# Kernel optimization log

Hardware: AMD Instinct MI355X
Metric: run time of the kernel (lower is better)

Reference implementation:

```python
import jax, jax.numpy as jnp
import numpy as np

N = 32          # agents_num
IN_DIM = 16     # node feature dim (excluding 2 pos cols)
HID = 128
HEADS = 4
OUT = 5
DUEL_H = 256
RADIUS = 0.3
LATENT = HID + HID * HEADS * 2  # 1152
BS = 128


def _lin(k, i, o):
    s = 1.0 / np.sqrt(i)
    return jax.random.uniform(k, (i, o), minval=-s, maxval=s, dtype=jnp.float32)


def setup_inputs() -> dict:
    key = jax.random.key(0)
    ks = jax.random.split(key, 16)
    pos = jax.random.uniform(ks[0], (BS, N, 2))
    feats = jax.random.normal(ks[1], (BS, N, IN_DIM))
    aidx = jax.random.randint(ks[2], (BS,), 0, N).astype(jnp.float32)
    node = jnp.concatenate([pos, feats], axis=-1).reshape(BS, N * (2 + IN_DIM))
    obs = jnp.concatenate([node, aidx[:, None]], axis=1)  # (BS, N*(2+IN_DIM)+1)
    return {
        "obs": obs,
        "enc_w1": _lin(ks[3], IN_DIM, HID), "enc_b1": jnp.zeros((HID,)),
        "enc_w2": _lin(ks[4], HID, HID), "enc_b2": jnp.zeros((HID,)),
        "wl1": _lin(ks[5], HID, HEADS * HID), "wr1": _lin(ks[6], HID, HEADS * HID),
        "att1": jax.random.normal(ks[7], (HEADS, HID)) * 0.1, "bias1": jnp.zeros((HEADS * HID,)),
        "wl2": _lin(ks[8], HID * HEADS, HEADS * HID), "wr2": _lin(ks[9], HID * HEADS, HEADS * HID),
        "att2": jax.random.normal(ks[10], (HEADS, HID)) * 0.1, "bias2": jnp.zeros((HEADS * HID,)),
        "q_w1": _lin(ks[11], LATENT, DUEL_H), "q_b1": jnp.zeros((DUEL_H,)),
        "q_w2": _lin(ks[12], DUEL_H, OUT), "q_b2": jnp.zeros((OUT,)),
        "v_w1": _lin(ks[13], LATENT, DUEL_H), "v_b1": jnp.zeros((DUEL_H,)),
        "v_w2": _lin(ks[14], DUEL_H, 1), "v_b2": jnp.zeros((1,)),
    }


def _gatv2(x, adj, wl, wr, att, bias):
    # Dense-masked GATv2 (PyG semantics: lin_l on source j, lin_r on target i,
    # leaky_relu(x_i + x_j) . att, softmax over neighbors j, aggregate lin_l(x_j)).
    bs, n, _ = x.shape
    gl = (x @ wl).reshape(bs, n, HEADS, HID)  # source transform
    gr = (x @ wr).reshape(bs, n, HEADS, HID)  # target transform
    e = jax.nn.leaky_relu(gr[:, :, None] + gl[:, None, :], 0.2)  # [b, i, j, h, c]
    logits = jnp.einsum('bijhc,hc->bijh', e, att)
    logits = jnp.where(adj[..., None], logits, -jnp.inf)  # diag always True (self loops)
    alpha = jax.nn.softmax(logits, axis=2)
    out = jnp.einsum('bijh,bjhc->bihc', alpha, gl).reshape(bs, n, HEADS * HID)
    return out + bias


def reference(obs, enc_w1, enc_b1, enc_w2, enc_b2,
              wl1, wr1, att1, bias1, wl2, wr2, att2, bias2,
              q_w1, q_b1, q_w2, q_b2, v_w1, v_b1, v_w2, v_b2):
    bs = obs.shape[0]
    node = obs[:, :-1].reshape(bs, N, 2 + IN_DIM)
    pos, feats = node[..., :2], node[..., 2:]
    aidx = jnp.clip(obs[:, -1], 0, N - 1).astype(jnp.int32)

    # radius_graph (per-graph, loop=False) + GATv2 add_self_loops => diag True
    d2 = jnp.sum((pos[:, :, None] - pos[:, None, :]) ** 2, axis=-1)  # [bs, N, N]
    adj = (d2 < RADIUS ** 2) | jnp.eye(N, dtype=bool)

    # encoder MLP then ReLU (as in forward)
    h = jax.nn.relu(feats @ enc_w1 + enc_b1)
    x = jax.nn.relu(h @ enc_w2 + enc_b2)  # [bs, N, HID]

    b = jnp.arange(bs)
    x1 = x[b, aidx]  # [bs, HID]

    x = jax.nn.relu(_gatv2(x, adj, wl1, wr1, att1, bias1))  # [bs, N, HID*HEADS]
    x2 = x[b, aidx]

    x = jax.nn.relu(_gatv2(x, adj, wl2, wr2, att2, bias2))
    x3 = x[b, aidx]

    x_cat = jnp.concatenate([x1, x2, x3], axis=1)  # [bs, LATENT]

    q = jax.nn.relu(x_cat @ q_w1 + q_b1) @ q_w2 + q_b2  # [bs, OUT]
    v = jax.nn.relu(x_cat @ v_w1 + v_b1) @ v_w2 + v_b2  # [bs, 1]
    return q - q.mean(axis=1, keepdims=True) + v
```

## Files before the change

kernel.cpp:

```cpp
#include <hip/hip_runtime.h>
#include <hip/hip_bf16.h>

typedef unsigned int uint_t;
typedef unsigned short ushort_t;
typedef __attribute__((ext_vector_type(8))) short short8;
typedef __attribute__((ext_vector_type(4))) float floatx4;

__device__ __forceinline__ float4 fma4(float4 a, float s, float4 w){
  a.x += s*w.x; a.y += s*w.y; a.z += s*w.z; a.w += s*w.w; return a;
}
__device__ __forceinline__ float4 relu4(float4 a){
  return make_float4(fmaxf(a.x,0.f),fmaxf(a.y,0.f),fmaxf(a.z,0.f),fmaxf(a.w,0.f));
}
__device__ __forceinline__ float comp4(float4 v, int k){
  return k==0? v.x : k==1? v.y : k==2? v.z : v.w;
}
__device__ __forceinline__ unsigned bf16rne(float f){
  unsigned u = __float_as_uint(f);
  return (u + 0x7fffu + ((u>>16)&1u)) >> 16;
}
__device__ __forceinline__ uint_t packbf(float f){
  unsigned hb = bf16rne(f);
  float hf = __uint_as_float(hb<<16);
  unsigned lb = bf16rne(f - hf);
  return (hb<<16) | lb;
}
__device__ __forceinline__ uint4 pack4(float4 v){
  uint4 u; u.x=packbf(v.x); u.y=packbf(v.y); u.z=packbf(v.z); u.w=packbf(v.w); return u;
}
__device__ __forceinline__ float unpk(uint_t u){
  return __uint_as_float(u & 0xffff0000u) + __uint_as_float(u<<16);
}


__global__ __launch_bounds__(256) void prep_kernel(
    const float* __restrict__ obs,
    const float* __restrict__ enc_w1, const float* __restrict__ enc_b1,
    const float* __restrict__ enc_w2, const float* __restrict__ enc_b2,
    const float* __restrict__ wl1, const float* __restrict__ wr1,
    const float* __restrict__ wl2,
    const float* __restrict__ q_w1, const float* __restrict__ v_w1,
    ushort_t* __restrict__ wl1Thi, ushort_t* __restrict__ wl1Tlo,
    ushort_t* __restrict__ wr1Thi, ushort_t* __restrict__ wr1Tlo,
    ushort_t* __restrict__ wl2Thi, ushort_t* __restrict__ wl2Tlo,
    ushort_t* __restrict__ qw1Thi, ushort_t* __restrict__ qw1Tlo,
    ushort_t* __restrict__ vw1Thi, ushort_t* __restrict__ vw1Tlo,
    uint_t* __restrict__ xpk,
    uint_t* __restrict__ xcatpk,
    unsigned* __restrict__ adjw, int* __restrict__ aiw)
{
  const int t = threadIdx.x, bid = blockIdx.x;
  if (bid >= 512){
    __shared__ float sm[32][33];
    const int cw = bid - 512;
    const float* in; ushort_t* ohi; ushort_t* olo; int K, N, tt;
    if (cw < 64)        { in=wl1;  ohi=wl1Thi; olo=wl1Tlo; K=128;  N=512; tt=cw; }
    else if (cw < 128)  { in=wr1;  ohi=wr1Thi; olo=wr1Tlo; K=128;  N=512; tt=cw-64; }
    else if (cw < 384)  { in=wl2;  ohi=wl2Thi; olo=wl2Tlo; K=512;  N=512; tt=cw-128; }
    else if (cw < 672)  { in=q_w1; ohi=qw1Thi; olo=qw1Tlo; K=1152; N=256; tt=cw-384; }
    else                { in=v_w1; ohi=vw1Thi; olo=vw1Tlo; K=1152; N=256; tt=cw-672; }
    const int ktiles = K>>5;
    const int kt = tt % ktiles, nt = tt / ktiles;
    const int r = t>>5, c = t&31;
    #pragma unroll
    for (int i=0;i<4;i++)
      sm[r+i*8][c] = in[(size_t)(kt*32 + r + i*8)*N + nt*32 + c];
    __syncthreads();
    #pragma unroll
    for (int i=0;i<4;i++){
      const int nl = r + i*8;
      const int n  = nt*32 + nl;
      const float f = sm[c][nl];
      const unsigned hb = bf16rne(f);
      const float hf = __uint_as_float(hb<<16);
      const unsigned lb = bf16rne(f - hf);
      const size_t off = (size_t)(n>>4)*(16*K) + (size_t)kt*512 + (size_t)(n&15)*32 + c;
      ohi[off] = (ushort_t)hb;
      olo[off] = (ushort_t)lb;
    }
    return;
  }
  __shared__ float s_pos[64];
  __shared__ float s_feats[128];
  __shared__ __align__(16) float s_h[8*132];
  __shared__ int s_ai;
  const int s = bid>>2, g = bid&3;
  const float* ob = obs + s*577;

  if (t==0){
    float a = ob[576];
    a = fminf(fmaxf(a, 0.f), 31.f);
    s_ai = (int)a;
    if (g==0) aiw[s] = (int)a;
  }
  if (t < 128){ const int n=t>>4, f=t&15; s_feats[t] = ob[(g*8+n)*18+2+f]; }
  if (g==0 && t>=128 && t<192){ const int u=t-128; s_pos[u] = ob[(u>>1)*18 + (u&1)]; }
  __syncthreads();

  if (g==0 && t < 32){
    const float px = s_pos[2*t], py = s_pos[2*t+1];
    const float R2 = 0.09f;
    unsigned mm = 0u;
    for (int j=0;j<32;j++){
      const float dx = __fsub_rn(px, s_pos[2*j]), dy = __fsub_rn(py, s_pos[2*j+1]);
      const float d2 = __fadd_rn(__fmul_rn(dx,dx), __fmul_rn(dy,dy));
      if (d2 <= R2 || j==t) mm |= (1u<<j);
    }
    adjw[s*32+t] = mm;
  }

  const int n = t>>5, c0 = (t&31)*4;
  {
    float4 a = *(const float4*)(enc_b1+c0);
    #pragma unroll
    for (int f=0; f<16; f++)
      a = fma4(a, s_feats[n*16+f], *(const float4*)(enc_w1 + f*128 + c0));
    *(float4*)&s_h[n*132+c0] = relu4(a);
  }
  __syncthreads();
  {
    float4 a = *(const float4*)(enc_b2+c0);
    for (int k=0;k<128;k+=4){
      const float4 hv = *(const float4*)&s_h[n*132+k];
      a = fma4(a, hv.x, *(const float4*)(enc_w2 + (k+0)*128 + c0));
      a = fma4(a, hv.y, *(const float4*)(enc_w2 + (k+1)*128 + c0));
      a = fma4(a, hv.z, *(const float4*)(enc_w2 + (k+2)*128 + c0));
      a = fma4(a, hv.w, *(const float4*)(enc_w2 + (k+3)*128 + c0));
    }
    a = relu4(a);
    const uint4 p = pack4(a);
    const int i = g*8 + n;
    uint_t* xp = xpk + (size_t)(s*2 + (i>>4))*2048 + (c0>>5)*512 + (i&15)*32 + (c0&31);
    *(uint4*)xp = p;
    if (i == s_ai){
      uint_t* xc = xcatpk + (size_t)(s>>4)*18432 + (c0>>5)*512 + (s&15)*32 + (c0&31);
      *(uint4*)xc = p;
    }
  }
}

__global__ __launch_bounds__(256) void pa1_kernel(
    const uint_t* __restrict__ xpk,
    const ushort_t* __restrict__ wl1Thi, const ushort_t* __restrict__ wl1Tlo,
    const ushort_t* __restrict__ wr1Thi, const ushort_t* __restrict__ wr1Tlo,
    const float* __restrict__ att, const float* __restrict__ bias,
    const unsigned* __restrict__ adjw, const int* __restrict__ aiw,
    uint_t* __restrict__ x2pk,
    uint_t* __restrict__ xcatpk)
{
  __shared__ __align__(16) float s_gl[32*132];
  __shared__ __align__(16) float s_gr[32*132];
  __shared__ __align__(16) float s_att[128];
  __shared__ __align__(16) float s_b[128];
  __shared__ float s_lg[32*33];
  __shared__ unsigned s_adj[32];
  const int t = threadIdx.x;
  const int s = blockIdx.x >> 2, h = blockIdx.x & 3;
  const int w = t>>6, lane = t&63, m = lane&15, quad = lane>>4;

  if (t < 128){ s_att[t] = att[h*128 + t]; s_b[t] = bias[h*128 + t]; }
  if (t >= 224) s_adj[t-224] = adjw[s*32 + (t-224)];
  const int ai = aiw[s];

  const ushort_t* Bhi = (w<2) ? wl1Thi : wr1Thi;
  const ushort_t* Blo = (w<2) ? wl1Tlo : wr1Tlo;
  const int nbase = h*8 + (w&1)*4;
  const uint_t* a0p = xpk + (size_t)(s*2+0)*2048 + m*32 + quad*8;
  const uint_t* a1p = xpk + (size_t)(s*2+1)*2048 + m*32 + quad*8;
  const ushort_t* bp0 = Bhi + (size_t)(nbase+0)*2048 + m*32 + quad*8;
  const ushort_t* bp1 = Bhi + (size_t)(nbase+1)*2048 + m*32 + quad*8;
  const ushort_t* bp2 = Bhi + (size_t)(nbase+2)*2048 + m*32 + quad*8;
  const ushort_t* bp3 = Bhi + (size_t)(nbase+3)*2048 + m*32 + quad*8;
  const size_t lod = (size_t)(Blo - Bhi);
  floatx4 acc[2][4];
  #pragma unroll
  for (int i=0;i<2;i++)
    #pragma unroll
    for (int j=0;j<4;j++) acc[i][j] = (floatx4){0.f,0.f,0.f,0.f};

  #pragma unroll
  for (int kc=0; kc<4; kc++){
    const uint4 u00 = *(const uint4*)(a0p + kc*512);
    const uint4 u01 = *(const uint4*)(a0p + kc*512 + 4);
    const uint4 u10 = *(const uint4*)(a1p + kc*512);
    const uint4 u11 = *(const uint4*)(a1p + kc*512 + 4);
    short8 ahi0, alo0, ahi1, alo1;
    ahi0[0]=(short)(u00.x>>16); alo0[0]=(short)u00.x;
    ahi0[1]=(short)(u00.y>>16); alo0[1]=(short)u00.y;
    ahi0[2]=(short)(u00.z>>16); alo0[2]=(short)u00.z;
    ahi0[3]=(short)(u00.w>>16); alo0[3]=(short)u00.w;
    ahi0[4]=(short)(u01.x>>16); alo0[4]=(short)u01.x;
    ahi0[5]=(short)(u01.y>>16); alo0[5]=(short)u01.y;
    ahi0[6]=(short)(u01.z>>16); alo0[6]=(short)u01.z;
    ahi0[7]=(short)(u01.w>>16); alo0[7]=(short)u01.w;
    ahi1[0]=(short)(u10.x>>16); alo1[0]=(short)u10.x;
    ahi1[1]=(short)(u10.y>>16); alo1[1]=(short)u10.y;
    ahi1[2]=(short)(u10.z>>16); alo1[2]=(short)u10.z;
    ahi1[3]=(short)(u10.w>>16); alo1[3]=(short)u10.w;
    ahi1[4]=(short)(u11.x>>16); alo1[4]=(short)u11.x;
    ahi1[5]=(short)(u11.y>>16); alo1[5]=(short)u11.y;
    ahi1[6]=(short)(u11.z>>16); alo1[6]=(short)u11.z;
    ahi1[7]=(short)(u11.w>>16); alo1[7]=(short)u11.w;
    const ushort_t* bps[4] = {bp0, bp1, bp2, bp3};
    #pragma unroll
    for (int nt=0; nt<4; nt++){
      const short8 bh = *(const short8*)(bps[nt] + kc*512);
      const short8 bl = *(const short8*)(bps[nt] + kc*512 + lod);
      acc[0][nt] = __builtin_amdgcn_mfma_f32_16x16x32_bf16(ahi0, bh, acc[0][nt], 0,0,0);
      acc[0][nt] = __builtin_amdgcn_mfma_f32_16x16x32_bf16(ahi0, bl, acc[0][nt], 0,0,0);
      acc[0][nt] = __builtin_amdgcn_mfma_f32_16x16x32_bf16(alo0, bh, acc[0][nt], 0,0,0);
      acc[1][nt] = __builtin_amdgcn_mfma_f32_16x16x32_bf16(ahi1, bh, acc[1][nt], 0,0,0);
      acc[1][nt] = __builtin_amdgcn_mfma_f32_16x16x32_bf16(ahi1, bl, acc[1][nt], 0,0,0);
      acc[1][nt] = __builtin_amdgcn_mfma_f32_16x16x32_bf16(alo1, bh, acc[1][nt], 0,0,0);
    }
  }
  {
    float* dst = (w<2) ? s_gl : s_gr;
    const int colbase = (w&1)*64;
    #pragma unroll
    for (int nt=0; nt<4; nt++){
      const int col = colbase + nt*16 + m;
      #pragma unroll
      for (int r=0;r<4;r++){
        dst[(quad*4+r)*132 + col]      = acc[0][nt][r];
        dst[(16+quad*4+r)*132 + col]   = acc[1][nt][r];
      }
    }
  }
  __syncthreads();

  {
    const int i = t>>3, jb = t&7;
    float lacc[4] = {0.f,0.f,0.f,0.f};
    for (int c=0;c<128;c+=4){
      const float4 g = *(const float4*)&s_gr[i*132+c];
      const float4 a = *(const float4*)&s_att[c];
      #pragma unroll
      for (int mm=0;mm<4;mm++){
        const float4 gj = *(const float4*)&s_gl[(jb+8*mm)*132 + c];
        float ex = g.x+gj.x; ex = fmaxf(ex, 0.2f*ex);
        float ey = g.y+gj.y; ey = fmaxf(ey, 0.2f*ey);
        float ez = g.z+gj.z; ez = fmaxf(ez, 0.2f*ez);
        float ew = g.w+gj.w; ew = fmaxf(ew, 0.2f*ew);
        lacc[mm] += ex*a.x + ey*a.y + ez*a.z + ew*a.w;
      }
    }
    #pragma unroll
    for (int mm=0;mm<4;mm++) s_lg[i*33 + jb + 8*mm] = lacc[mm];
  }
  __syncthreads();

  for (int rnd=0; rnd<4; rnd++){
    const int i = rnd*8 + (t>>5), j = t&31;
    const float lg = s_lg[i*33+j];
    const bool ok = (s_adj[i]>>j)&1u;
    float v = ok ? lg : -3.0e38f;
    #pragma unroll
    for (int d_=16; d_; d_>>=1) v = fmaxf(v, __shfl_xor(v, d_, 32));
    const float e = ok ? __expf(lg - v) : 0.f;
    float sum = e;
    #pragma unroll
    for (int d_=16; d_; d_>>=1) sum += __shfl_xor(sum, d_, 32);
    s_lg[i*33+j] = e / sum;
  }
  __syncthreads();

  {
    const int i = t>>3, c0 = (t&7)*16;
    float4 o0 = make_float4(0.f,0.f,0.f,0.f), o1 = o0, o2 = o0, o3 = o0;
    for (int j=0;j<32;j++){
      const float al = s_lg[i*33+j];
      o0 = fma4(o0, al, *(const float4*)&s_gl[j*132 + c0]);
      o1 = fma4(o1, al, *(const float4*)&s_gl[j*132 + c0 + 4]);
      o2 = fma4(o2, al, *(const float4*)&s_gl[j*132 + c0 + 8]);
      o3 = fma4(o3, al, *(const float4*)&s_gl[j*132 + c0 + 12]);
    }
    const float4 b0 = *(const float4*)&s_b[c0];
    const float4 b1 = *(const float4*)&s_b[c0+4];
    const float4 b2 = *(const float4*)&s_b[c0+8];
    const float4 b3 = *(const float4*)&s_b[c0+12];
    o0 = relu4(make_float4(o0.x+b0.x, o0.y+b0.y, o0.z+b0.z, o0.w+b0.w));
    o1 = relu4(make_float4(o1.x+b1.x, o1.y+b1.y, o1.z+b1.z, o1.w+b1.w));
    o2 = relu4(make_float4(o2.x+b2.x, o2.y+b2.y, o2.z+b2.z, o2.w+b2.w));
    o3 = relu4(make_float4(o3.x+b3.x, o3.y+b3.y, o3.z+b3.z, o3.w+b3.w));
    const uint4 p0 = pack4(o0), p1 = pack4(o1), p2 = pack4(o2), p3 = pack4(o3);
    const int kb = h*128 + c0;
    uint_t* xp = x2pk + (size_t)(s*2 + (i>>4))*8192 + (kb>>5)*512 + (i&15)*32 + (kb&31);
    *(uint4*)&xp[0]  = p0;
    *(uint4*)&xp[4]  = p1;
    *(uint4*)&xp[8]  = p2;
    *(uint4*)&xp[12] = p3;
    if (i == ai){
      const int kk = 128 + kb;
      uint_t* tp = xcatpk + (size_t)(s>>4)*18432 + (kk>>5)*512 + (s&15)*32 + (kk&31);
      *(uint4*)&tp[0]  = p0;
      *(uint4*)&tp[4]  = p1;
      *(uint4*)&tp[8]  = p2;
      *(uint4*)&tp[12] = p3;
    }
  }
}

__global__ __launch_bounds__(256) void pa2_kernel(
    const uint_t* __restrict__ x2pk,
    const ushort_t* __restrict__ wl2Thi, const ushort_t* __restrict__ wl2Tlo,
    const float* __restrict__ wr2f,
    const float* __restrict__ att2, const float* __restrict__ bias2,
    const unsigned* __restrict__ adjw, const int* __restrict__ aiw,
    uint_t* __restrict__ xcatpk)
{
  __shared__ __align__(16) float s_gl[32*132];
  __shared__ __align__(16) float s_xt[512];
  __shared__ __align__(16) float s_p2[2*128];
  __shared__ __align__(16) float s_at[128];
  __shared__ __align__(16) float s_bb[128];
  __shared__ float s_lg[32];
  __shared__ float s_al[32];
  const int t = threadIdx.x;
  const int s = blockIdx.x >> 2, h = blockIdx.x & 3;
  const int w = t>>6, lane = t&63, m = lane&15, quad = lane>>4;
  const int ai = aiw[s];
  const unsigned arow = adjw[s*32+ai];

  for (int e=t; e<512; e+=256){
    const int kk = 128 + e;
    s_xt[e] = unpk(xcatpk[(size_t)(s>>4)*18432 + (kk>>5)*512 + (s&15)*32 + (kk&31)]);
  }
  if (t < 128){ s_at[t] = att2[h*128+t]; s_bb[t] = bias2[h*128+t]; }
  __syncthreads();

  {
    const int c = t&127, half = t>>7;
    const float* wp = wr2f + (size_t)(half*256)*512 + h*128 + c;
    float ga = 0.f;
    #pragma unroll 8
    for (int k=0;k<256;k++) ga += s_xt[half*256 + k] * wp[(size_t)k*512];
    s_p2[half*128 + c] = ga;
  }

  const uint_t* a0p = x2pk + (size_t)(s*2+0)*8192 + m*32 + quad*8;
  const uint_t* a1p = x2pk + (size_t)(s*2+1)*8192 + m*32 + quad*8;
  const ushort_t* bq0 = wl2Thi + (size_t)(h*8 + w*2+0)*8192 + m*32 + quad*8;
  const ushort_t* bq1 = wl2Thi + (size_t)(h*8 + w*2+1)*8192 + m*32 + quad*8;
  const size_t lod = (size_t)(wl2Tlo - wl2Thi);
  floatx4 acc[2][2];
  #pragma unroll
  for (int i=0;i<2;i++){ acc[i][0] = (floatx4){0.f,0.f,0.f,0.f}; acc[i][1] = acc[i][0]; }
  for (int kc=0; kc<16; kc++){
    const uint4 u00 = *(const uint4*)(a0p + kc*512);
    const uint4 u01 = *(const uint4*)(a0p + kc*512 + 4);
    const uint4 u10 = *(const uint4*)(a1p + kc*512);
    const uint4 u11 = *(const uint4*)(a1p + kc*512 + 4);
    short8 ahi0, alo0, ahi1, alo1;
    ahi0[0]=(short)(u00.x>>16); alo0[0]=(short)u00.x;
    ahi0[1]=(short)(u00.y>>16); alo0[1]=(short)u00.y;
    ahi0[2]=(short)(u00.z>>16); alo0[2]=(short)u00.z;
    ahi0[3]=(short)(u00.w>>16); alo0[3]=(short)u00.w;
    ahi0[4]=(short)(u01.x>>16); alo0[4]=(short)u01.x;
    ahi0[5]=(short)(u01.y>>16); alo0[5]=(short)u01.y;
    ahi0[6]=(short)(u01.z>>16); alo0[6]=(short)u01.z;
    ahi0[7]=(short)(u01.w>>16); alo0[7]=(short)u01.w;
    ahi1[0]=(short)(u10.x>>16); alo1[0]=(short)u10.x;
    ahi1[1]=(short)(u10.y>>16); alo1[1]=(short)u10.y;
    ahi1[2]=(short)(u10.z>>16); alo1[2]=(short)u10.z;
    ahi1[3]=(short)(u10.w>>16); alo1[3]=(short)u10.w;
    ahi1[4]=(short)(u11.x>>16); alo1[4]=(short)u11.x;
    ahi1[5]=(short)(u11.y>>16); alo1[5]=(short)u11.y;
    ahi1[6]=(short)(u11.z>>16); alo1[6]=(short)u11.z;
    ahi1[7]=(short)(u11.w>>16); alo1[7]=(short)u11.w;
    {
      const short8 bh = *(const short8*)(bq0 + kc*512);
      const short8 bl = *(const short8*)(bq0 + kc*512 + lod);
      acc[0][0] = __builtin_amdgcn_mfma_f32_16x16x32_bf16(ahi0, bh, acc[0][0], 0,0,0);
      acc[0][0] = __builtin_amdgcn_mfma_f32_16x16x32_bf16(ahi0, bl, acc[0][0], 0,0,0);
      acc[0][0] = __builtin_amdgcn_mfma_f32_16x16x32_bf16(alo0, bh, acc[0][0], 0,0,0);
      acc[1][0] = __builtin_amdgcn_mfma_f32_16x16x32_bf16(ahi1, bh, acc[1][0], 0,0,0);
      acc[1][0] = __builtin_amdgcn_mfma_f32_16x16x32_bf16(ahi1, bl, acc[1][0], 0,0,0);
      acc[1][0] = __builtin_amdgcn_mfma_f32_16x16x32_bf16(alo1, bh, acc[1][0], 0,0,0);
    }
    {
      const short8 bh = *(const short8*)(bq1 + kc*512);
      const short8 bl = *(const short8*)(bq1 + kc*512 + lod);
      acc[0][1] = __builtin_amdgcn_mfma_f32_16x16x32_bf16(ahi0, bh, acc[0][1], 0,0,0);
      acc[0][1] = __builtin_amdgcn_mfma_f32_16x16x32_bf16(ahi0, bl, acc[0][1], 0,0,0);
      acc[0][1] = __builtin_amdgcn_mfma_f32_16x16x32_bf16(alo0, bh, acc[0][1], 0,0,0);
      acc[1][1] = __builtin_amdgcn_mfma_f32_16x16x32_bf16(ahi1, bh, acc[1][1], 0,0,0);
      acc[1][1] = __builtin_amdgcn_mfma_f32_16x16x32_bf16(ahi1, bl, acc[1][1], 0,0,0);
      acc[1][1] = __builtin_amdgcn_mfma_f32_16x16x32_bf16(alo1, bh, acc[1][1], 0,0,0);
    }
  }
  {
    const int colbase = w*32;
    #pragma unroll
    for (int nt=0; nt<2; nt++){
      const int col = colbase + nt*16 + m;
      #pragma unroll
      for (int r=0;r<4;r++){
        s_gl[(quad*4+r)*132 + col]    = acc[0][nt][r];
        s_gl[(16+quad*4+r)*132 + col] = acc[1][nt][r];
      }
    }
  }
  __syncthreads();

  if (t < 128) s_p2[t] = s_p2[t] + s_p2[128+t];
  __syncthreads();

  {
    const int j = t>>3, p = t&7;
    float sum = 0.f;
    #pragma unroll
    for (int q=0;q<4;q++){
      const int c = p*16 + q*4;
      const float4 g = *(const float4*)&s_gl[j*132 + c];
      const float4 r = *(const float4*)&s_p2[c];
      const float4 a = *(const float4*)&s_at[c];
      float e0 = r.x+g.x; e0 = fmaxf(e0, 0.2f*e0);
      float e1 = r.y+g.y; e1 = fmaxf(e1, 0.2f*e1);
      float e2 = r.z+g.z; e2 = fmaxf(e2, 0.2f*e2);
      float e3 = r.w+g.w; e3 = fmaxf(e3, 0.2f*e3);
      sum += e0*a.x + e1*a.y + e2*a.z + e3*a.w;
    }
    sum += __shfl_xor(sum,1,64);
    sum += __shfl_xor(sum,2,64);
    sum += __shfl_xor(sum,4,64);
    if (p==0) s_lg[j] = sum;
  }
  __syncthreads();
  if (t < 32){
    const float lg = s_lg[t];
    const bool ok = (arow>>t)&1u;
    float v = ok ? lg : -3.0e38f;
    #pragma unroll
    for (int d_=16; d_; d_>>=1) v = fmaxf(v, __shfl_xor(v, d_, 32));
    const float e = ok ? __expf(lg - v) : 0.f;
    float sm = e;
    #pragma unroll
    for (int d_=16; d_; d_>>=1) sm += __shfl_xor(sm, d_, 32);
    s_al[t] = e / sm;
  }
  __syncthreads();
  if (t < 128){
    float acc2 = 0.f;
    #pragma unroll 8
    for (int j=0;j<32;j++) acc2 += s_al[j] * s_gl[j*132 + t];
    const int kk = 640 + h*128 + t;
    xcatpk[(size_t)(s>>4)*18432 + (kk>>5)*512 + (s&15)*32 + (kk&31)]
        = packbf(fmaxf(acc2 + s_bb[t], 0.f));
  }
}

template<int KD>
__global__ __launch_bounds__(256) void mfma_gemm(
    const uint_t* __restrict__ A1, int rbs1,
    const ushort_t* __restrict__ B0hi, const ushort_t* __restrict__ B0lo,
    const ushort_t* __restrict__ B1hi, const ushort_t* __restrict__ B1lo,
    float* __restrict__ C0, float* __restrict__ C1,
    int nct1, int ctsplit)
{
  const int t = threadIdx.x;
  const int w = t>>6, lane = t&63;
  const int m = lane & 15, quad = lane >> 4;
  const int bid = blockIdx.x;
  const int rt = bid / nct1, ct = bid % nct1;
  const ushort_t* Bhi; const ushort_t* Blo; float* C; int cb;
  if (ct < ctsplit){ Bhi = B0hi; Blo = B0lo; C = C0; cb = ct*64; }
  else             { Bhi = B1hi; Blo = B1lo; C = C1; cb = (ct-ctsplit)*64; }
  const uint_t* ap = A1 + (size_t)(rt*4 + w)*rbs1 + m*32 + quad*8;
  const ushort_t* bp0 = Bhi + (size_t)((cb>>4)+0)*(16*KD) + m*32 + quad*8;
  const ushort_t* bp1 = Bhi + (size_t)((cb>>4)+1)*(16*KD) + m*32 + quad*8;
  const ushort_t* bp2 = Bhi + (size_t)((cb>>4)+2)*(16*KD) + m*32 + quad*8;
  const ushort_t* bp3 = Bhi + (size_t)((cb>>4)+3)*(16*KD) + m*32 + quad*8;
  const size_t lod = (size_t)(Blo - Bhi);
  floatx4 acc[4];
  #pragma unroll
  for (int i=0;i<4;i++) acc[i] = (floatx4){0.f,0.f,0.f,0.f};

  for (int kc=0; kc<KD/32; kc++){
    const uint4 ua0 = *(const uint4*)(ap);
    const uint4 ua1 = *(const uint4*)(ap+4);
    ap += 512;
    short8 ahi, alo;
    ahi[0]=(short)(ua0.x>>16); alo[0]=(short)(ua0.x);
    ahi[1]=(short)(ua0.y>>16); alo[1]=(short)(ua0.y);
    ahi[2]=(short)(ua0.z>>16); alo[2]=(short)(ua0.z);
    ahi[3]=(short)(ua0.w>>16); alo[3]=(short)(ua0.w);
    ahi[4]=(short)(ua1.x>>16); alo[4]=(short)(ua1.x);
    ahi[5]=(short)(ua1.y>>16); alo[5]=(short)(ua1.y);
    ahi[6]=(short)(ua1.z>>16); alo[6]=(short)(ua1.z);
    ahi[7]=(short)(ua1.w>>16); alo[7]=(short)(ua1.w);
    {
      const short8 bh = *(const short8*)(bp0);
      const short8 bl = *(const short8*)(bp0 + lod);
      acc[0] = __builtin_amdgcn_mfma_f32_16x16x32_bf16(ahi, bh, acc[0], 0,0,0);
      acc[0] = __builtin_amdgcn_mfma_f32_16x16x32_bf16(ahi, bl, acc[0], 0,0,0);
      acc[0] = __builtin_amdgcn_mfma_f32_16x16x32_bf16(alo, bh, acc[0], 0,0,0);
      bp0 += 512;
    }
    {
      const short8 bh = *(const short8*)(bp1);
      const short8 bl = *(const short8*)(bp1 + lod);
      acc[1] = __builtin_amdgcn_mfma_f32_16x16x32_bf16(ahi, bh, acc[1], 0,0,0);
      acc[1] = __builtin_amdgcn_mfma_f32_16x16x32_bf16(ahi, bl, acc[1], 0,0,0);
      acc[1] = __builtin_amdgcn_mfma_f32_16x16x32_bf16(alo, bh, acc[1], 0,0,0);
      bp1 += 512;
    }
    {
      const short8 bh = *(const short8*)(bp2);
      const short8 bl = *(const short8*)(bp2 + lod);
      acc[2] = __builtin_amdgcn_mfma_f32_16x16x32_bf16(ahi, bh, acc[2], 0,0,0);
      acc[2] = __builtin_amdgcn_mfma_f32_16x16x32_bf16(ahi, bl, acc[2], 0,0,0);
      acc[2] = __builtin_amdgcn_mfma_f32_16x16x32_bf16(alo, bh, acc[2], 0,0,0);
      bp2 += 512;
    }
    {
      const short8 bh = *(const short8*)(bp3);
      const short8 bl = *(const short8*)(bp3 + lod);
      acc[3] = __builtin_amdgcn_mfma_f32_16x16x32_bf16(ahi, bh, acc[3], 0,0,0);
      acc[3] = __builtin_amdgcn_mfma_f32_16x16x32_bf16(ahi, bl, acc[3], 0,0,0);
      acc[3] = __builtin_amdgcn_mfma_f32_16x16x32_bf16(alo, bh, acc[3], 0,0,0);
      bp3 += 512;
    }
  }
  const int crow0 = rt*64 + w*16 + quad*4;
  #pragma unroll
  for (int nt2=0; nt2<4; nt2++){
    const int col = cb + nt2*16 + m;
    #pragma unroll
    for (int r=0;r<4;r++)
      C[(size_t)(crow0 + r)*512 + col] = acc[nt2][r];
  }
}

__global__ __launch_bounds__(256) void heads2_kernel(
    const float* __restrict__ Ch,
    const float* __restrict__ q_b1, const float* __restrict__ q_w2, const float* __restrict__ q_b2,
    const float* __restrict__ v_b1, const float* __restrict__ v_w2, const float* __restrict__ v_b2,
    float* __restrict__ out)
{
  __shared__ float s_p[4*6];
  const int t = threadIdx.x, s = blockIdx.x;
  const float hq = fmaxf(Ch[(size_t)s*512 + t]       + q_b1[t], 0.f);
  const float hv = fmaxf(Ch[(size_t)s*512 + 256 + t] + v_b1[t], 0.f);
  float p[6];
  #pragma unroll
  for (int o=0;o<5;o++) p[o] = hq * q_w2[t*5+o];
  p[5] = hv * v_w2[t];
  #pragma unroll
  for (int d_=32; d_; d_>>=1){
    #pragma unroll
    for (int o=0;o<6;o++) p[o] += __shfl_xor(p[o], d_, 64);
  }
  const int w = t>>6, lane = t&63;
  if (lane==0){
    #pragma unroll
    for (int o=0;o<6;o++) s_p[w*6+o] = p[o];
  }
  __syncthreads();
  if (t < 6) s_p[t] = s_p[t] + s_p[6+t] + s_p[12+t] + s_p[18+t];
  __syncthreads();
  if (t < 5){
    const float q0 = s_p[0]+q_b2[0], q1 = s_p[1]+q_b2[1], q2 = s_p[2]+q_b2[2],
                q3 = s_p[3]+q_b2[3], q4 = s_p[4]+q_b2[4];
    const float mean = (q0+q1+q2+q3+q4) / 5.0f;
    const float v = s_p[5] + v_b2[0];
    const float qt = (t==0?q0:t==1?q1:t==2?q2:t==3?q3:q4);
    out[s*5+t] = qt - mean + v;
  }
}

extern "C" void kernel_launch(void* const* d_in, const int* in_sizes, int n_in,
                              void* d_out, int out_size, void* d_ws, size_t ws_size,
                              hipStream_t stream) {
  (void)n_in; (void)out_size; (void)ws_size;
  const float* obs    = (const float*)d_in[0];
  const float* enc_w1 = (const float*)d_in[1];
  const float* enc_b1 = (const float*)d_in[2];
  const float* enc_w2 = (const float*)d_in[3];
  const float* enc_b2 = (const float*)d_in[4];
  const float* wl1    = (const float*)d_in[5];
  const float* wr1    = (const float*)d_in[6];
  const float* att1   = (const float*)d_in[7];
  const float* bias1  = (const float*)d_in[8];
  const float* wl2    = (const float*)d_in[9];
  const float* wr2    = (const float*)d_in[10];
  const float* att2   = (const float*)d_in[11];
  const float* bias2  = (const float*)d_in[12];
  const float* q_w1   = (const float*)d_in[13];
  const float* q_b1   = (const float*)d_in[14];
  const float* q_w2   = (const float*)d_in[15];
  const float* q_b2   = (const float*)d_in[16];
  const float* v_w1   = (const float*)d_in[17];
  const float* v_b1   = (const float*)d_in[18];
  const float* v_w2   = (const float*)d_in[19];
  const float* v_b2   = (const float*)d_in[20];

  char* ws = (char*)d_ws;
  uint_t*   x_pk    = (uint_t*)  (ws + 0);
  uint_t*   xcat_pk = (uint_t*)  (ws + 2097152);
  unsigned* adjw    = (unsigned*)(ws + 2686976);
  int*      aiw     = (int*)     (ws + 2703360);
  uint_t*   x2_pk   = (uint_t*)  (ws + 2703872);
  ushort_t* wl1Thi  = (ushort_t*)(ws + 11092480);
  ushort_t* wl1Tlo  = (ushort_t*)(ws + 11223552);
  ushort_t* wr1Thi  = (ushort_t*)(ws + 11354624);
  ushort_t* wr1Tlo  = (ushort_t*)(ws + 11485696);
  ushort_t* wl2Thi  = (ushort_t*)(ws + 11616768);
  ushort_t* wl2Tlo  = (ushort_t*)(ws + 12141056);
  ushort_t* qw1Thi  = (ushort_t*)(ws + 12665344);
  ushort_t* qw1Tlo  = (ushort_t*)(ws + 13255168);
  ushort_t* vw1Thi  = (ushort_t*)(ws + 13844992);
  ushort_t* vw1Tlo  = (ushort_t*)(ws + 14434816);
  float*    headsC  = (float*)   (ws + 15024640);

  const int bs = in_sizes[0] / 577;

  prep_kernel<<<512 + 960, 256, 0, stream>>>(obs, enc_w1, enc_b1, enc_w2, enc_b2,
      wl1, wr1, wl2, q_w1, v_w1,
      wl1Thi, wl1Tlo, wr1Thi, wr1Tlo, wl2Thi, wl2Tlo,
      qw1Thi, qw1Tlo, vw1Thi, vw1Tlo,
      x_pk, xcat_pk, adjw, aiw);

  pa1_kernel<<<bs*4, 256, 0, stream>>>(x_pk, wl1Thi, wl1Tlo, wr1Thi, wr1Tlo,
                                       att1, bias1, adjw, aiw, x2_pk, xcat_pk);

  pa2_kernel<<<bs*4, 256, 0, stream>>>(x2_pk, wl2Thi, wl2Tlo, wr2,
                                       att2, bias2, adjw, aiw, xcat_pk);

  mfma_gemm<1152><<<16, 256, 0, stream>>>(xcat_pk, 18432,
      qw1Thi, qw1Tlo, vw1Thi, vw1Tlo, headsC, headsC + 256, 8, 4);

  heads2_kernel<<<bs, 256, 0, stream>>>(headsC, q_b1, q_w2, q_b2, v_b1, v_w2, v_b2,
                                        (float*)d_out);
}
```

Before: 197.0 us.

## Split GAT projection K dimension across 512-thread blocks with shared-memory reduction

Both GAT attention kernels move from 256 to 512 threads per block. The extra waves each take half of the K range of the MFMA projection and write partial results into extra shared buffers, which are then summed. The later attention and aggregation phases are also re-split across more threads. The goal is more parallelism and latency hiding per block, at the cost of more shared memory (lower occupancy), an extra reduction pass, and an extra barrier.

```diff
diff --git a/kernel.cpp b/kernel.cpp
--- a/kernel.cpp
+++ b/kernel.cpp
@@ -11,9 +11,6 @@
 }
 __device__ __forceinline__ float4 relu4(float4 a){
   return make_float4(fmaxf(a.x,0.f),fmaxf(a.y,0.f),fmaxf(a.z,0.f),fmaxf(a.w,0.f));
-}
-__device__ __forceinline__ float comp4(float4 v, int k){
-  return k==0? v.x : k==1? v.y : k==2? v.z : v.w;
 }
 __device__ __forceinline__ unsigned bf16rne(float f){
   unsigned u = __float_as_uint(f);
@@ -31,6 +28,15 @@
 __device__ __forceinline__ float unpk(uint_t u){
   return __uint_as_float(u & 0xffff0000u) + __uint_as_float(u<<16);
 }
+#define UNPACK8(u0,u1,hi,lo) \
+  hi[0]=(short)(u0.x>>16); lo[0]=(short)u0.x; \
+  hi[1]=(short)(u0.y>>16); lo[1]=(short)u0.y; \
+  hi[2]=(short)(u0.z>>16); lo[2]=(short)u0.z; \
+  hi[3]=(short)(u0.w>>16); lo[3]=(short)u0.w; \
+  hi[4]=(short)(u1.x>>16); lo[4]=(short)u1.x; \
+  hi[5]=(short)(u1.y>>16); lo[5]=(short)u1.y; \
+  hi[6]=(short)(u1.z>>16); lo[6]=(short)u1.z; \
+  hi[7]=(short)(u1.w>>16); lo[7]=(short)u1.w;
 
 
 __global__ __launch_bounds__(256) void prep_kernel(
@@ -45,8 +51,7 @@
     ushort_t* __restrict__ wl2Thi, ushort_t* __restrict__ wl2Tlo,
     ushort_t* __restrict__ qw1Thi, ushort_t* __restrict__ qw1Tlo,
     ushort_t* __restrict__ vw1Thi, ushort_t* __restrict__ vw1Tlo,
-    uint_t* __restrict__ xpk,
-    uint_t* __restrict__ xcatpk,
+    uint_t* __restrict__ xpk, uint_t* __restrict__ xcatpk,
     unsigned* __restrict__ adjw, int* __restrict__ aiw)
 {
   const int t = threadIdx.x, bid = blockIdx.x;
@@ -139,17 +144,18 @@
   }
 }
 
-__global__ __launch_bounds__(256) void pa1_kernel(
+__global__ __launch_bounds__(512) void pa1_kernel(
     const uint_t* __restrict__ xpk,
     const ushort_t* __restrict__ wl1Thi, const ushort_t* __restrict__ wl1Tlo,
     const ushort_t* __restrict__ wr1Thi, const ushort_t* __restrict__ wr1Tlo,
     const float* __restrict__ att, const float* __restrict__ bias,
     const unsigned* __restrict__ adjw, const int* __restrict__ aiw,
-    uint_t* __restrict__ x2pk,
-    uint_t* __restrict__ xcatpk)
+    uint_t* __restrict__ x2pk, uint_t* __restrict__ xcatpk)
 {
   __shared__ __align__(16) float s_gl[32*132];
+  __shared__ __align__(16) float s_glB[32*132];
   __shared__ __align__(16) float s_gr[32*132];
+  __shared__ __align__(16) float s_grB[32*132];
   __shared__ __align__(16) float s_att[128];
   __shared__ __align__(16) float s_b[128];
   __shared__ float s_lg[32*33];
@@ -157,20 +163,22 @@
   const int t = threadIdx.x;
   const int s = blockIdx.x >> 2, h = blockIdx.x & 3;
   const int w = t>>6, lane = t&63, m = lane&15, quad = lane>>4;
+  const int ww = w&3, khalf = w>>2;
 
   if (t < 128){ s_att[t] = att[h*128 + t]; s_b[t] = bias[h*128 + t]; }
-  if (t >= 224) s_adj[t-224] = adjw[s*32 + (t-224)];
+  if (t >= 224 && t < 256) s_adj[t-224] = adjw[s*32 + (t-224)];
   const int ai = aiw[s];
 
-  const ushort_t* Bhi = (w<2) ? wl1Thi : wr1Thi;
-  const ushort_t* Blo = (w<2) ? wl1Tlo : wr1Tlo;
-  const int nbase = h*8 + (w&1)*4;
-  const uint_t* a0p = xpk + (size_t)(s*2+0)*2048 + m*32 + quad*8;
-  const uint_t* a1p = xpk + (size_t)(s*2+1)*2048 + m*32 + quad*8;
-  const ushort_t* bp0 = Bhi + (size_t)(nbase+0)*2048 + m*32 + quad*8;
-  const ushort_t* bp1 = Bhi + (size_t)(nbase+1)*2048 + m*32 + quad*8;
-  const ushort_t* bp2 = Bhi + (size_t)(nbase+2)*2048 + m*32 + quad*8;
-  const ushort_t* bp3 = Bhi + (size_t)(nbase+3)*2048 + m*32 + quad*8;
+  const ushort_t* Bhi = (ww<2) ? wl1Thi : wr1Thi;
+  const ushort_t* Blo = (ww<2) ? wl1Tlo : wr1Tlo;
+  const int nbase = h*8 + (ww&1)*4;
+  const int kcb = khalf*2;
+  const uint_t* a0p = xpk + (size_t)(s*2+0)*2048 + m*32 + quad*8 + kcb*512;
+  const uint_t* a1p = xpk + (size_t)(s*2+1)*2048 + m*32 + quad*8 + kcb*512;
+  const ushort_t* bp0 = Bhi + (size_t)(nbase+0)*2048 + m*32 + quad*8 + kcb*512;
+  const ushort_t* bp1 = Bhi + (size_t)(nbase+1)*2048 + m*32 + quad*8 + kcb*512;
+  const ushort_t* bp2 = Bhi + (size_t)(nbase+2)*2048 + m*32 + quad*8 + kcb*512;
+  const ushort_t* bp3 = Bhi + (size_t)(nbase+3)*2048 + m*32 + quad*8 + kcb*512;
   const size_t lod = (size_t)(Blo - Bhi);
   floatx4 acc[2][4];
   #pragma unroll
@@ -179,28 +187,14 @@
     for (int j=0;j<4;j++) acc[i][j] = (floatx4){0.f,0.f,0.f,0.f};
 
   #pragma unroll
-  for (int kc=0; kc<4; kc++){
+  for (int kc=0; kc<2; kc++){
     const uint4 u00 = *(const uint4*)(a0p + kc*512);
     const uint4 u01 = *(const uint4*)(a0p + kc*512 + 4);
     const uint4 u10 = *(const uint4*)(a1p + kc*512);
     const uint4 u11 = *(const uint4*)(a1p + kc*512 + 4);
     short8 ahi0, alo0, ahi1, alo1;
-    ahi0[0]=(short)(u00.x>>16); alo0[0]=(short)u00.x;
-    ahi0[1]=(short)(u00.y>>16); alo0[1]=(short)u00.y;
-    ahi0[2]=(short)(u00.z>>16); alo0[2]=(short)u00.z;
-    ahi0[3]=(short)(u00.w>>16); alo0[3]=(short)u00.w;
-    ahi0[4]=(short)(u01.x>>16); alo0[4]=(short)u01.x;
-    ahi0[5]=(short)(u01.y>>16); alo0[5]=(short)u01.y;
-    ahi0[6]=(short)(u01.z>>16); alo0[6]=(short)u01.z;
-    ahi0[7]=(short)(u01.w>>16); alo0[7]=(short)u01.w;
-    ahi1[0]=(short)(u10.x>>16); alo1[0]=(short)u10.x;
-    ahi1[1]=(short)(u10.y>>16); alo1[1]=(short)u10.y;
-    ahi1[2]=(short)(u10.z>>16); alo1[2]=(short)u10.z;
-    ahi1[3]=(short)(u10.w>>16); alo1[3]=(short)u10.w;
-    ahi1[4]=(short)(u11.x>>16); alo1[4]=(short)u11.x;
-    ahi1[5]=(short)(u11.y>>16); alo1[5]=(short)u11.y;
-    ahi1[6]=(short)(u11.z>>16); alo1[6]=(short)u11.z;
-    ahi1[7]=(short)(u11.w>>16); alo1[7]=(short)u11.w;
+    UNPACK8(u00,u01,ahi0,alo0)
+    UNPACK8(u10,u11,ahi1,alo1)
     const ushort_t* bps[4] = {bp0, bp1, bp2, bp3};
     #pragma unroll
     for (int nt=0; nt<4; nt++){
@@ -215,8 +209,8 @@
     }
   }
   {
-    float* dst = (w<2) ? s_gl : s_gr;
-    const int colbase = (w&1)*64;
+    float* dst = (ww<2) ? (khalf ? s_glB : s_gl) : (khalf ? s_grB : s_gr);
+    const int colbase = (ww&1)*64;
     #pragma unroll
     for (int nt=0; nt<4; nt++){
       const int col = colbase + nt*16 + m;
@@ -228,16 +222,21 @@
     }
   }
   __syncthreads();
-
-  {
-    const int i = t>>3, jb = t&7;
-    float lacc[4] = {0.f,0.f,0.f,0.f};
+  for (int e=t; e<32*132; e+=512){
+    s_gl[e] += s_glB[e];
+    s_gr[e] += s_grB[e];
+  }
+  __syncthreads();
+
+  {
+    const int i = t>>4, jb = t&15;
+    float lacc[2] = {0.f,0.f};
     for (int c=0;c<128;c+=4){
       const float4 g = *(const float4*)&s_gr[i*132+c];
       const float4 a = *(const float4*)&s_att[c];
       #pragma unroll
-      for (int mm=0;mm<4;mm++){
-        const float4 gj = *(const float4*)&s_gl[(jb+8*mm)*132 + c];
+      for (int mm=0;mm<2;mm++){
+        const float4 gj = *(const float4*)&s_gl[(jb+16*mm)*132 + c];
         float ex = g.x+gj.x; ex = fmaxf(ex, 0.2f*ex);
         float ey = g.y+gj.y; ey = fmaxf(ey, 0.2f*ey);
         float ez = g.z+gj.z; ez = fmaxf(ez, 0.2f*ez);
@@ -245,13 +244,14 @@
         lacc[mm] += ex*a.x + ey*a.y + ez*a.z + ew*a.w;
       }
     }
-    #pragma unroll
-    for (int mm=0;mm<4;mm++) s_lg[i*33 + jb + 8*mm] = lacc[mm];
-  }
-  __syncthreads();
-
-  for (int rnd=0; rnd<4; rnd++){
-    const int i = rnd*8 + (t>>5), j = t&31;
+    s_lg[i*33 + jb]      = lacc[0];
+    s_lg[i*33 + jb + 16] = lacc[1];
+  }
+  __syncthreads();
+
+  #pragma unroll
+  for (int rnd=0; rnd<2; rnd++){
+    const int i = rnd*16 + (t>>5), j = t&31;
     const float lg = s_lg[i*33+j];
     const bool ok = (s_adj[i]>>j)&1u;
     float v = ok ? lg : -3.0e38f;
@@ -266,42 +266,32 @@
   __syncthreads();
 
   {
-    const int i = t>>3, c0 = (t&7)*16;
-    float4 o0 = make_float4(0.f,0.f,0.f,0.f), o1 = o0, o2 = o0, o3 = o0;
+    const int i = t>>4, c0 = (t&15)*8;
+    float4 o0 = make_float4(0.f,0.f,0.f,0.f), o1 = o0;
     for (int j=0;j<32;j++){
       const float al = s_lg[i*33+j];
       o0 = fma4(o0, al, *(const float4*)&s_gl[j*132 + c0]);
       o1 = fma4(o1, al, *(const float4*)&s_gl[j*132 + c0 + 4]);
-      o2 = fma4(o2, al, *(const float4*)&s_gl[j*132 + c0 + 8]);
-      o3 = fma4(o3, al, *(const float4*)&s_gl[j*132 + c0 + 12]);
     }
     const float4 b0 = *(const float4*)&s_b[c0];
     const float4 b1 = *(const float4*)&s_b[c0+4];
-    const float4 b2 = *(const float4*)&s_b[c0+8];
-    const float4 b3 = *(const float4*)&s_b[c0+12];
     o0 = relu4(make_float4(o0.x+b0.x, o0.y+b0.y, o0.z+b0.z, o0.w+b0.w));
     o1 = relu4(make_float4(o1.x+b1.x, o1.y+b1.y, o1.z+b1.z, o1.w+b1.w));
-    o2 = relu4(make_float4(o2.x+b2.x, o2.y+b2.y, o2.z+b2.z, o2.w+b2.w));
-    o3 = relu4(make_float4(o3.x+b3.x, o3.y+b3.y, o3.z+b3.z, o3.w+b3.w));
-    const uint4 p0 = pack4(o0), p1 = pack4(o1), p2 = pack4(o2), p3 = pack4(o3);
+    const uint4 p0 = pack4(o0), p1 = pack4(o1);
     const int kb = h*128 + c0;
     uint_t* xp = x2pk + (size_t)(s*2 + (i>>4))*8192 + (kb>>5)*512 + (i&15)*32 + (kb&31);
-    *(uint4*)&xp[0]  = p0;
-    *(uint4*)&xp[4]  = p1;
-    *(uint4*)&xp[8]  = p2;
-    *(uint4*)&xp[12] = p3;
+    *(uint4*)&xp[0] = p0;
+    *(uint4*)&xp[4] = p1;
     if (i == ai){
       const int kk = 128 + kb;
       uint_t* tp = xcatpk + (size_t)(s>>4)*18432 + (kk>>5)*512 + (s&15)*32 + (kk&31);
-      *(uint4*)&tp[0]  = p0;
-      *(uint4*)&tp[4]  = p1;
-      *(uint4*)&tp[8]  = p2;
-      *(uint4*)&tp[12] = p3;
-    }
-  }
-}
-
-__global__ __launch_bounds__(256) void pa2_kernel(
+      *(uint4*)&tp[0] = p0;
+      *(uint4*)&tp[4] = p1;
+    }
+  }
+}
+
+__global__ __launch_bounds__(512) void pa2_kernel(
     const uint_t* __restrict__ x2pk,
     const ushort_t* __restrict__ wl2Thi, const ushort_t* __restrict__ wl2Tlo,
     const float* __restrict__ wr2f,
@@ -310,8 +300,9 @@
     uint_t* __restrict__ xcatpk)
 {
   __shared__ __align__(16) float s_gl[32*132];
+  __shared__ __align__(16) float s_glB[32*132];
   __shared__ __align__(16) float s_xt[512];
-  __shared__ __align__(16) float s_p2[2*128];
+  __shared__ __align__(16) float s_p2[4*128];
   __shared__ __align__(16) float s_at[128];
   __shared__ __align__(16) float s_bb[128];
   __shared__ float s_lg[32];
@@ -319,55 +310,44 @@
   const int t = threadIdx.x;
   const int s = blockIdx.x >> 2, h = blockIdx.x & 3;
   const int w = t>>6, lane = t&63, m = lane&15, quad = lane>>4;
+  const int ww = w&3, khalf = w>>2;
   const int ai = aiw[s];
   const unsigned arow = adjw[s*32+ai];
 
-  for (int e=t; e<512; e+=256){
-    const int kk = 128 + e;
-    s_xt[e] = unpk(xcatpk[(size_t)(s>>4)*18432 + (kk>>5)*512 + (s&15)*32 + (kk&31)]);
+  {
+    const int kk = 128 + t;
+    s_xt[t] = unpk(xcatpk[(size_t)(s>>4)*18432 + (kk>>5)*512 + (s&15)*32 + (kk&31)]);
   }
   if (t < 128){ s_at[t] = att2[h*128+t]; s_bb[t] = bias2[h*128+t]; }
   __syncthreads();
 
   {
-    const int c = t&127, half = t>>7;
-    const float* wp = wr2f + (size_t)(half*256)*512 + h*128 + c;
+    const int c = t&127, q4 = t>>7;
+    const float* wp = wr2f + (size_t)(q4*128)*512 + h*128 + c;
     float ga = 0.f;
     #pragma unroll 8
-    for (int k=0;k<256;k++) ga += s_xt[half*256 + k] * wp[(size_t)k*512];
-    s_p2[half*128 + c] = ga;
-  }
-
-  const uint_t* a0p = x2pk + (size_t)(s*2+0)*8192 + m*32 + quad*8;
-  const uint_t* a1p = x2pk + (size_t)(s*2+1)*8192 + m*32 + quad*8;
-  const ushort_t* bq0 = wl2Thi + (size_t)(h*8 + w*2+0)*8192 + m*32 + quad*8;
-  const ushort_t* bq1 = wl2Thi + (size_t)(h*8 + w*2+1)*8192 + m*32 + quad*8;
+    for (int k=0;k<128;k++) ga += s_xt[q4*128 + k] * wp[(size_t)k*512];
+    s_p2[q4*128 + c] = ga;
+  }
+
+  const int kcb = khalf*8;
+  const uint_t* a0p = x2pk + (size_t)(s*2+0)*8192 + m*32 + quad*8 + kcb*512;
+  const uint_t* a1p = x2pk + (size_t)(s*2+1)*8192 + m*32 + quad*8 + kcb*512;
+  const ushort_t* bq0 = wl2Thi + (size_t)(h*8 + ww*2+0)*8192 + m*32 + quad*8 + kcb*512;
+  const ushort_t* bq1 = wl2Thi + (size_t)(h*8 + ww*2+1)*8192 + m*32 + quad*8 + kcb*512;
   const size_t lod = (size_t)(wl2Tlo - wl2Thi);
   floatx4 acc[2][2];
   #pragma unroll
   for (int i=0;i<2;i++){ acc[i][0] = (floatx4){0.f,0.f,0.f,0.f}; acc[i][1] = acc[i][0]; }
-  for (int kc=0; kc<16; kc++){
+  #pragma unroll 4
+  for (int kc=0; kc<8; kc++){
     const uint4 u00 = *(const uint4*)(a0p + kc*512);
     const uint4 u01 = *(const uint4*)(a0p + kc*512 + 4);
     const uint4 u10 = *(const uint4*)(a1p + kc*512);
     const uint4 u11 = *(const uint4*)(a1p + kc*512 + 4);
     short8 ahi0, alo0, ahi1, alo1;
-    ahi0[0]=(short)(u00.x>>16); alo0[0]=(short)u00.x;
-    ahi0[1]=(short)(u00.y>>16); alo0[1]=(short)u00.y;
-    ahi0[2]=(short)(u00.z>>16); alo0[2]=(short)u00.z;
-    ahi0[3]=(short)(u00.w>>16); alo0[3]=(short)u00.w;
-    ahi0[4]=(short)(u01.x>>16); alo0[4]=(short)u01.x;
-    ahi0[5]=(short)(u01.y>>16); alo0[5]=(short)u01.y;
-    ahi0[6]=(short)(u01.z>>16); alo0[6]=(short)u01.z;
-    ahi0[7]=(short)(u01.w>>16); alo0[7]=(short)u01.w;
-    ahi1[0]=(short)(u10.x>>16); alo1[0]=(short)u10.x;
-    ahi1[1]=(short)(u10.y>>16); alo1[1]=(short)u10.y;
-    ahi1[2]=(short)(u10.z>>16); alo1[2]=(short)u10.z;
-    ahi1[3]=(short)(u10.w>>16); alo1[3]=(short)u10.w;
-    ahi1[4]=(short)(u11.x>>16); alo1[4]=(short)u11.x;
-    ahi1[5]=(short)(u11.y>>16); alo1[5]=(short)u11.y;
-    ahi1[6]=(short)(u11.z>>16); alo1[6]=(short)u11.z;
-    ahi1[7]=(short)(u11.w>>16); alo1[7]=(short)u11.w;
+    UNPACK8(u00,u01,ahi0,alo0)
+    UNPACK8(u10,u11,ahi1,alo1)
     {
       const short8 bh = *(const short8*)(bq0 + kc*512);
       const short8 bl = *(const short8*)(bq0 + kc*512 + lod);
@@ -390,23 +370,24 @@
     }
   }
   {
-    const int colbase = w*32;
+    float* dst = khalf ? s_glB : s_gl;
+    const int colbase = ww*32;
     #pragma unroll
     for (int nt=0; nt<2; nt++){
       const int col = colbase + nt*16 + m;
       #pragma unroll
       for (int r=0;r<4;r++){
-        s_gl[(quad*4+r)*132 + col]    = acc[0][nt][r];
-        s_gl[(16+quad*4+r)*132 + col] = acc[1][nt][r];
+        dst[(quad*4+r)*132 + col]    = acc[0][nt][r];
+        dst[(16+quad*4+r)*132 + col] = acc[1][nt][r];
       }
     }
   }
   __syncthreads();
-
-  if (t < 128) s_p2[t] = s_p2[t] + s_p2[128+t];
-  __syncthreads();
-
-  {
+  for (int e=t; e<32*132; e+=512) s_gl[e] += s_glB[e];
+  if (t < 128) s_p2[t] = s_p2[t] + s_p2[128+t] + s_p2[256+t] + s_p2[384+t];
+  __syncthreads();
+
+  if (t < 256){
     const int j = t>>3, p = t&7;
     float sum = 0.f;
     #pragma unroll
@@ -481,14 +462,7 @@
     const uint4 ua1 = *(const uint4*)(ap+4);
     ap += 512;
     short8 ahi, alo;
-    ahi[0]=(short)(ua0.x>>16); alo[0]=(short)(ua0.x);
-    ahi[1]=(short)(ua0.y>>16); alo[1]=(short)(ua0.y);
-    ahi[2]=(short)(ua0.z>>16); alo[2]=(short)(ua0.z);
-    ahi[3]=(short)(ua0.w>>16); alo[3]=(short)(ua0.w);
-    ahi[4]=(short)(ua1.x>>16); alo[4]=(short)(ua1.x);
-    ahi[5]=(short)(ua1.y>>16); alo[5]=(short)(ua1.y);
-    ahi[6]=(short)(ua1.z>>16); alo[6]=(short)(ua1.z);
-    ahi[7]=(short)(ua1.w>>16); alo[7]=(short)(ua1.w);
+    UNPACK8(ua0,ua1,ahi,alo)
     {
       const short8 bh = *(const short8*)(bp0);
       const short8 bl = *(const short8*)(bp0 + lod);
@@ -621,10 +595,10 @@
       qw1Thi, qw1Tlo, vw1Thi, vw1Tlo,
       x_pk, xcat_pk, adjw, aiw);
 
-  pa1_kernel<<<bs*4, 256, 0, stream>>>(x_pk, wl1Thi, wl1Tlo, wr1Thi, wr1Tlo,
+  pa1_kernel<<<bs*4, 512, 0, stream>>>(x_pk, wl1Thi, wl1Tlo, wr1Thi, wr1Tlo,
                                        att1, bias1, adjw, aiw, x2_pk, xcat_pk);
 
-  pa2_kernel<<<bs*4, 256, 0, stream>>>(x2_pk, wl2Thi, wl2Tlo, wr2,
+  pa2_kernel<<<bs*4, 512, 0, stream>>>(x2_pk, wl2Thi, wl2Tlo, wr2,
                                        att2, bias2, adjw, aiw, xcat_pk);
 
   mfma_gemm<1152><<<16, 256, 0, stream>>>(xcat_pk, 18432,
```

Result: faster. 191.8 us (-2.6%).
